# Optimization experiments

Measured on AMD Instinct MI355X. Metric: run time of the kernel, lower is better.

## Reference

```python
import jax, jax.numpy as jnp
import numpy as np

B, T, IN, H, HORIZON = 1024, 256, 128, 128, 24


def setup_inputs() -> dict:
    key = jax.random.key(0)
    ks = jax.random.split(key, 10)
    def init(k, shape, fan_in):
        return jax.random.normal(k, shape, jnp.float32) / np.sqrt(fan_in)
    return {
        "x": jax.random.normal(ks[0], (B, T, IN), jnp.float32),
        # haiku hk.GRU params: w_i [in, 3H], w_h [H, 3H], b [3H]
        "w_i": init(ks[1], (IN, 3 * H), IN),
        "w_h": init(ks[2], (H, 3 * H), H),
        "b": jnp.zeros((3 * H,), jnp.float32),
        # MLP: single Linear H -> 4H (no final activation)
        "mlp_w": init(ks[3], (H, 4 * H), H),
        "mlp_b": jnp.zeros((4 * H,), jnp.float32),
        # fc: Linear(T*4H -> H) after flatten
        "fc_w": init(ks[4], (T * 4 * H, H), T * 4 * H),
        "fc_b": jnp.zeros((H,), jnp.float32),
        # fc_out: Linear(H -> horizon)
        "out_w": init(ks[5], (H, HORIZON), H),
        "out_b": jnp.zeros((HORIZON,), jnp.float32),
    }


def reference(x, w_i, w_h, b, mlp_w, mlp_b, fc_w, fc_b, out_w, out_b):
    h_dim = w_h.shape[0]
    w_h_zr, w_h_a = w_h[:, : 2 * h_dim], w_h[:, 2 * h_dim :]
    b_zr, b_a = b[: 2 * h_dim], b[2 * h_dim :]

    def step(h, xt):  # h: [B,H], xt: [B,IN]  (haiku hk.GRU math)
        gx = xt @ w_i  # [B,3H]
        zr = jax.nn.sigmoid(gx[:, : 2 * h_dim] + h @ w_h_zr + b_zr)
        z, r = zr[:, :h_dim], zr[:, h_dim:]
        a = jnp.tanh(gx[:, 2 * h_dim :] + (r * h) @ w_h_a + b_a)
        h_new = (1.0 - z) * h + z * a
        return h_new, h_new

    h0 = jnp.zeros((x.shape[0], h_dim), x.dtype)
    _, ys = jax.lax.scan(step, h0, jnp.swapaxes(x, 0, 1))  # ys: [T,B,H]
    ys = jnp.swapaxes(ys, 0, 1)  # [B,T,H]
    y = ys @ mlp_w + mlp_b  # [B,T,4H]
    y = y.reshape(x.shape[0], -1)  # [B, T*4H]
    y = y @ fc_w + fc_b  # [B,H]
    return y @ out_w + out_b  # [B,horizon]
```

## Files before the change

### kernel.cpp

```cpp
#include <hip/hip_runtime.h>
#include <hip/hip_bf16.h>

typedef __bf16 bf16x8 __attribute__((ext_vector_type(8)));
typedef float f32x4 __attribute__((ext_vector_type(4)));

#define MFMA16(A, B, C) __builtin_amdgcn_mfma_f32_16x16x32_bf16((A), (B), (C), 0, 0, 0)

namespace {
constexpr int kT = 256, kIN = 128, kHZ = 24;
constexpr int kRB = 16;
}

__device__ __forceinline__ float fsig(float v) {
  float e = __builtin_amdgcn_exp2f(-1.44269504088896340736f * v);
  return __builtin_amdgcn_rcpf(1.0f + e);
}
__device__ __forceinline__ float ftanh(float v) {
  float e = __builtin_amdgcn_exp2f(2.88539008177792681472f * v);
  return 1.0f - 2.0f * __builtin_amdgcn_rcpf(e + 1.0f);
}

__global__ __launch_bounds__(256, 1) void gru_main(
    const float* __restrict__ x, const float* __restrict__ w_i,
    const float* __restrict__ w_h, const float* __restrict__ bias,
    const __bf16* __restrict__ Nfrag, const float* __restrict__ cvec,
    float* __restrict__ out)
{
  const int tid = threadIdx.x;
  const int w = tid >> 6;
  const int l = tid & 63;
  const int lrow = l & 15;
  const int lg = l >> 4;
  const int b0 = blockIdx.x * kRB;

  __shared__ float h_f32[16][132];
  __shared__ float zbuf[16][132];
  __shared__ __align__(16) __bf16 h_bf[16 * 128];
  __shared__ __align__(16) __bf16 rh_bf[16 * 128];
  __shared__ __align__(16) float red[4][64][4];

  for (int i = tid; i < 16 * 132; i += 256) { ((float*)h_f32)[i] = 0.0f; ((float*)zbuf)[i] = 0.0f; }
  for (int i = tid; i < 16 * 128; i += 256) { h_bf[i] = (__bf16)0.0f; rh_bf[i] = (__bf16)0.0f; }

  bf16x8 Wzr[8][4];
  bf16x8 Wa[8][2];
#pragma unroll
  for (int kc = 0; kc < 8; ++kc) {
#pragma unroll
    for (int nt = 0; nt < 4; ++nt) {
      const int col = w * 64 + nt * 16 + lrow;
      bf16x8 f;
#pragma unroll
      for (int e = 0; e < 8; ++e) {
        const int k = kc * 32 + lg * 8 + e;
        const float v = (k < 128) ? w_i[k * 384 + col] : w_h[(k - 128) * 384 + col];
        f[e] = (__bf16)v;
      }
      Wzr[kc][nt] = f;
    }
  }
#pragma unroll
  for (int kc = 0; kc < 8; ++kc) {
#pragma unroll
    for (int nt = 0; nt < 2; ++nt) {
      const int col = 256 + w * 32 + nt * 16 + lrow;
      bf16x8 f;
#pragma unroll
      for (int e = 0; e < 8; ++e) {
        const int k = kc * 32 + lg * 8 + e;
        const float v = (k < 128) ? w_i[k * 384 + col] : w_h[(k - 128) * 384 + col];
        f[e] = (__bf16)v;
      }
      Wa[kc][nt] = f;
    }
  }

  float bz[4], ba[2];
#pragma unroll
  for (int nt = 0; nt < 4; ++nt) bz[nt] = bias[w * 64 + nt * 16 + lrow];
#pragma unroll
  for (int nt = 0; nt < 2; ++nt) ba[nt] = bias[256 + w * 32 + nt * 16 + lrow];

  const int kcA = (w & 2);
  const __bf16* nbase = Nfrag + (size_t)(w & 1) * 512 + (size_t)l * 8;

  const float* xbase = x + ((size_t)(b0 + lrow)) * kT * kIN + lg * 8;

  f32x4 oacc = {0.f, 0.f, 0.f, 0.f};
  bf16x8 nfA, nfB;
#pragma unroll
  for (int e = 0; e < 8; ++e) { nfA[e] = (__bf16)0.0f; nfB[e] = (__bf16)0.0f; }
  bf16x8 xf[4], hf[4], rf[4];
  float4 xpre[8];

#pragma unroll
  for (int kc = 0; kc < 4; ++kc) {
    const float4* p = (const float4*)(xbase + kc * 32);
    xpre[2 * kc] = p[0];
    xpre[2 * kc + 1] = p[1];
  }
#pragma unroll
  for (int kc = 0; kc < 4; ++kc) {
    bf16x8 f;
    f[0] = (__bf16)xpre[2*kc].x;   f[1] = (__bf16)xpre[2*kc].y;
    f[2] = (__bf16)xpre[2*kc].z;   f[3] = (__bf16)xpre[2*kc].w;
    f[4] = (__bf16)xpre[2*kc+1].x; f[5] = (__bf16)xpre[2*kc+1].y;
    f[6] = (__bf16)xpre[2*kc+1].z; f[7] = (__bf16)xpre[2*kc+1].w;
    xf[kc] = f;
  }

  __syncthreads();

#pragma unroll 1
  for (int t = 0; t < kT; ++t) {
#pragma unroll
    for (int kc = 0; kc < 4; ++kc) {
      const int idx = (lrow * 128 + kc * 32 + lg * 8) ^ ((lrow & 7) << 3);
      hf[kc] = *(const bf16x8*)(h_bf + idx);
    }
    if (t > 0) {
      bf16x8 hA, hB;
      if (w & 2) { hA = hf[2]; hB = hf[3]; } else { hA = hf[0]; hB = hf[1]; }
      oacc = MFMA16(hA, nfA, oacc);
      oacc = MFMA16(hB, nfB, oacc);
    }
    {
      const __bf16* np = nbase + (size_t)t * 4096 + (size_t)kcA * 1024;
      nfA = *(const bf16x8*)(np);
      nfB = *(const bf16x8*)(np + 1024);
    }
    {
      const int tn = (t < kT - 1) ? (t + 1) : t;
#pragma unroll
      for (int kc = 0; kc < 4; ++kc) {
        const float4* p = (const float4*)(xbase + (size_t)tn * kIN + kc * 32);
        xpre[2 * kc] = p[0];
        xpre[2 * kc + 1] = p[1];
      }
    }
    f32x4 acc1[4];
#pragma unroll
    for (int nt = 0; nt < 4; ++nt) { f32x4 a = {bz[nt], bz[nt], bz[nt], bz[nt]}; acc1[nt] = a; }
#pragma unroll
    for (int kc = 0; kc < 4; ++kc) {
#pragma unroll
      for (int nt = 0; nt < 4; ++nt) acc1[nt] = MFMA16(xf[kc], Wzr[kc][nt], acc1[nt]);
    }
#pragma unroll
    for (int kc = 0; kc < 4; ++kc) {
#pragma unroll
      for (int nt = 0; nt < 4; ++nt) acc1[nt] = MFMA16(hf[kc], Wzr[kc + 4][nt], acc1[nt]);
    }
    if (w < 2) {
#pragma unroll
      for (int nt = 0; nt < 4; ++nt) {
#pragma unroll
        for (int r = 0; r < 4; ++r) {
          const int row = lg * 4 + r;
          const int col = w * 64 + nt * 16 + lrow;
          zbuf[row][col] = fsig(acc1[nt][r]);
        }
      }
    } else {
#pragma unroll
      for (int nt = 0; nt < 4; ++nt) {
#pragma unroll
        for (int r = 0; r < 4; ++r) {
          const int row = lg * 4 + r;
          const int cr = (w - 2) * 64 + nt * 16 + lrow;
          const float s = fsig(acc1[nt][r]);
          const float rh = s * h_f32[row][cr];
          rh_bf[(row * 128 + cr) ^ ((row & 7) << 3)] = (__bf16)rh;
        }
      }
    }
    __syncthreads();
#pragma unroll
    for (int kc = 0; kc < 4; ++kc) {
      const int idx = (lrow * 128 + kc * 32 + lg * 8) ^ ((lrow & 7) << 3);
      rf[kc] = *(const bf16x8*)(rh_bf + idx);
    }
    f32x4 acc2[2];
#pragma unroll
    for (int nt = 0; nt < 2; ++nt) { f32x4 a = {ba[nt], ba[nt], ba[nt], ba[nt]}; acc2[nt] = a; }
#pragma unroll
    for (int kc = 0; kc < 4; ++kc) {
#pragma unroll
      for (int nt = 0; nt < 2; ++nt) acc2[nt] = MFMA16(xf[kc], Wa[kc][nt], acc2[nt]);
    }
#pragma unroll
    for (int kc = 0; kc < 4; ++kc) {
#pragma unroll
      for (int nt = 0; nt < 2; ++nt) acc2[nt] = MFMA16(rf[kc], Wa[kc + 4][nt], acc2[nt]);
    }
#pragma unroll
    for (int kc = 0; kc < 4; ++kc) {
      bf16x8 f;
      f[0] = (__bf16)xpre[2*kc].x;   f[1] = (__bf16)xpre[2*kc].y;
      f[2] = (__bf16)xpre[2*kc].z;   f[3] = (__bf16)xpre[2*kc].w;
      f[4] = (__bf16)xpre[2*kc+1].x; f[5] = (__bf16)xpre[2*kc+1].y;
      f[6] = (__bf16)xpre[2*kc+1].z; f[7] = (__bf16)xpre[2*kc+1].w;
      xf[kc] = f;
    }
#pragma unroll
    for (int nt = 0; nt < 2; ++nt) {
#pragma unroll
      for (int r = 0; r < 4; ++r) {
        const int row = lg * 4 + r;
        const int col = w * 32 + nt * 16 + lrow;
        const float a = ftanh(acc2[nt][r]);
        const float hold = h_f32[row][col];
        const float z = zbuf[row][col];
        const float hn = fmaf(z, a - hold, hold);
        h_f32[row][col] = hn;
        h_bf[(row * 128 + col) ^ ((row & 7) << 3)] = (__bf16)hn;
      }
    }
    __syncthreads();
  }

#pragma unroll
  for (int kc = 0; kc < 4; ++kc) {
    const int idx = (lrow * 128 + kc * 32 + lg * 8) ^ ((lrow & 7) << 3);
    hf[kc] = *(const bf16x8*)(h_bf + idx);
  }
  {
    bf16x8 hA, hB;
    if (w & 2) { hA = hf[2]; hB = hf[3]; } else { hA = hf[0]; hB = hf[1]; }
    oacc = MFMA16(hA, nfA, oacc);
    oacc = MFMA16(hB, nfB, oacc);
  }
  *(f32x4*)(&red[w][l][0]) = oacc;
  __syncthreads();
  if (w < 2) {
#pragma unroll
    for (int r = 0; r < 4; ++r) {
      const int row = lg * 4 + r;
      const int col = w * 16 + lrow;
      if (col < kHZ) {
        const float v = red[w][l][r] + red[w + 2][l][r] + cvec[col];
        out[(size_t)(b0 + row) * kHZ + col] = v;
      }
    }
  }
}

__global__ __launch_bounds__(256) void nprep(
    const float* __restrict__ mlp_w, const float* __restrict__ fc_w,
    const float* __restrict__ out_w, __bf16* __restrict__ Nfrag)
{
  const int t = blockIdx.x;
  const int tid = threadIdx.x;
  __shared__ __align__(16) float Q[512 * 24];
  __shared__ __align__(16) float obuf[4096];

  float* ow = obuf;
  for (int i = tid; i < 128 * 24; i += 256) ow[i] = out_w[i];
  __syncthreads();

  for (int i = tid; i < 512; i += 256) {
    const float* rowp = fc_w + ((size_t)t * 512 + i) * 128;
    float q[24];
#pragma unroll
    for (int j = 0; j < 24; ++j) q[j] = 0.0f;
    auto acc_m = [&](float rv, int m) {
      const float4* owp = (const float4*)(ow + m * 24);
      const float4 o0 = owp[0], o1 = owp[1], o2 = owp[2];
      const float4 o3 = owp[3], o4 = owp[4], o5 = owp[5];
      q[0]  = fmaf(rv, o0.x, q[0]);  q[1]  = fmaf(rv, o0.y, q[1]);
      q[2]  = fmaf(rv, o0.z, q[2]);  q[3]  = fmaf(rv, o0.w, q[3]);
      q[4]  = fmaf(rv, o1.x, q[4]);  q[5]  = fmaf(rv, o1.y, q[5]);
      q[6]  = fmaf(rv, o1.z, q[6]);  q[7]  = fmaf(rv, o1.w, q[7]);
      q[8]  = fmaf(rv, o2.x, q[8]);  q[9]  = fmaf(rv, o2.y, q[9]);
      q[10] = fmaf(rv, o2.z, q[10]); q[11] = fmaf(rv, o2.w, q[11]);
      q[12] = fmaf(rv, o3.x, q[12]); q[13] = fmaf(rv, o3.y, q[13]);
      q[14] = fmaf(rv, o3.z, q[14]); q[15] = fmaf(rv, o3.w, q[15]);
      q[16] = fmaf(rv, o4.x, q[16]); q[17] = fmaf(rv, o4.y, q[17]);
      q[18] = fmaf(rv, o4.z, q[18]); q[19] = fmaf(rv, o4.w, q[19]);
      q[20] = fmaf(rv, o5.x, q[20]); q[21] = fmaf(rv, o5.y, q[21]);
      q[22] = fmaf(rv, o5.z, q[22]); q[23] = fmaf(rv, o5.w, q[23]);
    };
#pragma unroll 4
    for (int m4 = 0; m4 < 32; ++m4) {
      const float4 rv = *(const float4*)(rowp + m4 * 4);
      acc_m(rv.x, m4 * 4 + 0);
      acc_m(rv.y, m4 * 4 + 1);
      acc_m(rv.z, m4 * 4 + 2);
      acc_m(rv.w, m4 * 4 + 3);
    }
#pragma unroll
    for (int j = 0; j < 24; ++j) Q[i * 24 + j] = q[j];
  }
  __syncthreads();

  {
    const int i = tid & 127;
    const int jh = tid >> 7;
    const float* mrow = mlp_w + (size_t)i * 512;
    float q[12];
#pragma unroll
    for (int j = 0; j < 12; ++j) q[j] = 0.0f;
    auto acc_k = [&](float mv, int k) {
      const float* qrow = Q + (size_t)k * 24 + jh * 12;
      const float4 q0 = *(const float4*)(qrow);
      const float4 q1 = *(const float4*)(qrow + 4);
      const float4 q2 = *(const float4*)(qrow + 8);
      q[0]  = fmaf(mv, q0.x, q[0]);  q[1]  = fmaf(mv, q0.y, q[1]);
      q[2]  = fmaf(mv, q0.z, q[2]);  q[3]  = fmaf(mv, q0.w, q[3]);
      q[4]  = fmaf(mv, q1.x, q[4]);  q[5]  = fmaf(mv, q1.y, q[5]);
      q[6]  = fmaf(mv, q1.z, q[6]);  q[7]  = fmaf(mv, q1.w, q[7]);
      q[8]  = fmaf(mv, q2.x, q[8]);  q[9]  = fmaf(mv, q2.y, q[9]);
      q[10] = fmaf(mv, q2.z, q[10]); q[11] = fmaf(mv, q2.w, q[11]);
    };
#pragma unroll 2
    for (int k4 = 0; k4 < 128; ++k4) {
      const float4 mv = *(const float4*)(mrow + k4 * 4);
      acc_k(mv.x, k4 * 4 + 0);
      acc_k(mv.y, k4 * 4 + 1);
      acc_k(mv.z, k4 * 4 + 2);
      acc_k(mv.w, k4 * 4 + 3);
    }
    float* Nb = obuf;
#pragma unroll
    for (int j = 0; j < 12; ++j) Nb[i * 32 + jh * 12 + j] = q[j];
  }
  for (int idx = tid; idx < 128 * 8; idx += 256) obuf[(idx >> 3) * 32 + 24 + (idx & 7)] = 0.0f;
  __syncthreads();

  {
    const float* Nb = obuf;
#pragma unroll
    for (int u = 0; u < 16; ++u) {
      const int f = tid * 16 + u;
      const int e = f & 7;
      const int lane = (f >> 3) & 63;
      const int nt = (f >> 9) & 1;
      const int kc = f >> 10;
      const int k = kc * 32 + (lane >> 4) * 8 + e;
      const int colj = nt * 16 + (lane & 15);
      Nfrag[(size_t)t * 4096 + f] = (__bf16)Nb[k * 32 + colj];
    }
  }
}

__global__ __launch_bounds__(256) void bias_partial(
    const float* __restrict__ mlp_b, const float* __restrict__ fc_w,
    float* __restrict__ partial)
{
  const int r0 = blockIdx.x;
  const int tid = threadIdx.x;
  const int m = tid & 127;
  const int g = tid >> 7;
  __shared__ int anynz;
  if (tid == 0) anynz = 0;
  __syncthreads();
  {
    int nz = 0;
    for (int i = tid; i < 512; i += 256) nz |= (mlp_b[i] != 0.0f) ? 1 : 0;
    if (nz) atomicOr(&anynz, 1);
  }
  __syncthreads();
  float acc = 0.0f;
  if (anynz) {
    for (int i = g; i < 512; i += 2)
      acc = fmaf(mlp_b[i], fc_w[((size_t)r0 * 512 + i) * 128 + m], acc);
  }
  __shared__ float sred[2][128];
  sred[g][m] = acc;
  __syncthreads();
  if (g == 0) partial[r0 * 128 + m] = sred[0][m] + sred[1][m];
}

__global__ __launch_bounds__(128) void bias_final(
    const float* __restrict__ fc_b, const float* __restrict__ out_b,
    const float* __restrict__ out_w, const float* __restrict__ partial,
    float* __restrict__ cvec)
{
  const int m = threadIdx.x;
  float s = fc_b[m];
  for (int r0 = 0; r0 < 256; ++r0) s += partial[r0 * 128 + m];
  __shared__ float sm[128];
  sm[m] = s;
  __syncthreads();
  if (m < kHZ) {
    float c = out_b[m];
    for (int k = 0; k < 128; ++k) c = fmaf(sm[k], out_w[k * kHZ + m], c);
    cvec[m] = c;
  }
}

extern "C" void kernel_launch(void* const* d_in, const int* in_sizes, int n_in,
                              void* d_out, int out_size, void* d_ws, size_t ws_size,
                              hipStream_t stream) {
  (void)in_sizes; (void)n_in; (void)out_size; (void)ws_size;
  const float* x     = (const float*)d_in[0];
  const float* w_i   = (const float*)d_in[1];
  const float* w_h   = (const float*)d_in[2];
  const float* bias  = (const float*)d_in[3];
  const float* mlp_w = (const float*)d_in[4];
  const float* mlp_b = (const float*)d_in[5];
  const float* fc_w  = (const float*)d_in[6];
  const float* fc_b  = (const float*)d_in[7];
  const float* out_w = (const float*)d_in[8];
  const float* out_b = (const float*)d_in[9];
  float* out = (float*)d_out;

  __bf16* Nfrag  = (__bf16*)d_ws;
  float* partial = (float*)((char*)d_ws + (size_t)256 * 4096 * 2);
  float* cvec    = (float*)((char*)d_ws + (size_t)256 * 4096 * 2 + 256 * 128 * 4);

  nprep<<<256, 256, 0, stream>>>(mlp_w, fc_w, out_w, Nfrag);
  bias_partial<<<256, 256, 0, stream>>>(mlp_b, fc_w, partial);
  bias_final<<<1, 128, 0, stream>>>(fc_b, out_b, out_w, partial, cvec);
  gru_main<<<64, 256, 0, stream>>>(x, w_i, w_h, bias, Nfrag, cvec, out);
}
```

Before: 715.2 us.

## Split GRU recurrence across 8 waves per block and use lighter LDS barriers

Doubles the workgroup from 4 to 8 wavefronts so each wave computes half as many gate columns per timestep. This shortens the serial per-step MFMA chain on the latency-bound recurrence, and the output projection is split four ways across k-chunks and reduced at the end. The __syncthreads calls inside the step loop are replaced by an explicit lgkmcnt wait plus s_barrier. In exchange, each step synchronises more waves, and every wave still loads the full h and x fragments, so redundant LDS and global traffic grows.

```diff
diff --git a/kernel.cpp b/kernel.cpp
--- a/kernel.cpp
+++ b/kernel.cpp
@@ -5,6 +5,11 @@
 typedef float f32x4 __attribute__((ext_vector_type(4)));
 
 #define MFMA16(A, B, C) __builtin_amdgcn_mfma_f32_16x16x32_bf16((A), (B), (C), 0, 0, 0)
+
+#define BARRIER_LDS() do { \
+    asm volatile("s_waitcnt lgkmcnt(0)" ::: "memory"); \
+    __builtin_amdgcn_s_barrier(); \
+  } while (0)
 
 namespace {
 constexpr int kT = 256, kIN = 128, kHZ = 24;
@@ -20,7 +25,7 @@
   return 1.0f - 2.0f * __builtin_amdgcn_rcpf(e + 1.0f);
 }
 
-__global__ __launch_bounds__(256, 1) void gru_main(
+__global__ __launch_bounds__(512, 2) void gru_main(
     const float* __restrict__ x, const float* __restrict__ w_i,
     const float* __restrict__ w_h, const float* __restrict__ bias,
     const __bf16* __restrict__ Nfrag, const float* __restrict__ cvec,
@@ -37,18 +42,18 @@
   __shared__ float zbuf[16][132];
   __shared__ __align__(16) __bf16 h_bf[16 * 128];
   __shared__ __align__(16) __bf16 rh_bf[16 * 128];
-  __shared__ __align__(16) float red[4][64][4];
-
-  for (int i = tid; i < 16 * 132; i += 256) { ((float*)h_f32)[i] = 0.0f; ((float*)zbuf)[i] = 0.0f; }
-  for (int i = tid; i < 16 * 128; i += 256) { h_bf[i] = (__bf16)0.0f; rh_bf[i] = (__bf16)0.0f; }
-
-  bf16x8 Wzr[8][4];
-  bf16x8 Wa[8][2];
+  __shared__ __align__(16) float red[8][64][4];
+
+  for (int i = tid; i < 16 * 132; i += 512) { ((float*)h_f32)[i] = 0.0f; ((float*)zbuf)[i] = 0.0f; }
+  for (int i = tid; i < 16 * 128; i += 512) { h_bf[i] = (__bf16)0.0f; rh_bf[i] = (__bf16)0.0f; }
+
+  bf16x8 Wzr[8][2];
+  bf16x8 Wa[8];
 #pragma unroll
   for (int kc = 0; kc < 8; ++kc) {
 #pragma unroll
-    for (int nt = 0; nt < 4; ++nt) {
-      const int col = w * 64 + nt * 16 + lrow;
+    for (int nt = 0; nt < 2; ++nt) {
+      const int col = w * 32 + nt * 16 + lrow;
       bf16x8 f;
 #pragma unroll
       for (int e = 0; e < 8; ++e) {
@@ -61,35 +66,32 @@
   }
 #pragma unroll
   for (int kc = 0; kc < 8; ++kc) {
-#pragma unroll
-    for (int nt = 0; nt < 2; ++nt) {
-      const int col = 256 + w * 32 + nt * 16 + lrow;
-      bf16x8 f;
-#pragma unroll
-      for (int e = 0; e < 8; ++e) {
-        const int k = kc * 32 + lg * 8 + e;
-        const float v = (k < 128) ? w_i[k * 384 + col] : w_h[(k - 128) * 384 + col];
-        f[e] = (__bf16)v;
-      }
-      Wa[kc][nt] = f;
-    }
-  }
-
-  float bz[4], ba[2];
-#pragma unroll
-  for (int nt = 0; nt < 4; ++nt) bz[nt] = bias[w * 64 + nt * 16 + lrow];
-#pragma unroll
-  for (int nt = 0; nt < 2; ++nt) ba[nt] = bias[256 + w * 32 + nt * 16 + lrow];
-
-  const int kcA = (w & 2);
-  const __bf16* nbase = Nfrag + (size_t)(w & 1) * 512 + (size_t)l * 8;
+    const int col = 256 + w * 16 + lrow;
+    bf16x8 f;
+#pragma unroll
+    for (int e = 0; e < 8; ++e) {
+      const int k = kc * 32 + lg * 8 + e;
+      const float v = (k < 128) ? w_i[k * 384 + col] : w_h[(k - 128) * 384 + col];
+      f[e] = (__bf16)v;
+    }
+    Wa[kc] = f;
+  }
+
+  float bz[2], ba;
+#pragma unroll
+  for (int nt = 0; nt < 2; ++nt) bz[nt] = bias[w * 32 + nt * 16 + lrow];
+  ba = bias[256 + w * 16 + lrow];
+
+  const int kcA = w & 3;
+  const int ntA = w >> 2;
+  const __bf16* nbase = Nfrag + (size_t)kcA * 1024 + (size_t)ntA * 512 + (size_t)l * 8;
 
   const float* xbase = x + ((size_t)(b0 + lrow)) * kT * kIN + lg * 8;
 
   f32x4 oacc = {0.f, 0.f, 0.f, 0.f};
-  bf16x8 nfA, nfB;
-#pragma unroll
-  for (int e = 0; e < 8; ++e) { nfA[e] = (__bf16)0.0f; nfB[e] = (__bf16)0.0f; }
+  bf16x8 nf;
+#pragma unroll
+  for (int e = 0; e < 8; ++e) nf[e] = (__bf16)0.0f;
   bf16x8 xf[4], hf[4], rf[4];
   float4 xpre[8];
 
@@ -113,22 +115,6 @@
 
 #pragma unroll 1
   for (int t = 0; t < kT; ++t) {
-#pragma unroll
-    for (int kc = 0; kc < 4; ++kc) {
-      const int idx = (lrow * 128 + kc * 32 + lg * 8) ^ ((lrow & 7) << 3);
-      hf[kc] = *(const bf16x8*)(h_bf + idx);
-    }
-    if (t > 0) {
-      bf16x8 hA, hB;
-      if (w & 2) { hA = hf[2]; hB = hf[3]; } else { hA = hf[0]; hB = hf[1]; }
-      oacc = MFMA16(hA, nfA, oacc);
-      oacc = MFMA16(hB, nfB, oacc);
-    }
-    {
-      const __bf16* np = nbase + (size_t)t * 4096 + (size_t)kcA * 1024;
-      nfA = *(const bf16x8*)(np);
-      nfB = *(const bf16x8*)(np + 1024);
-    }
     {
       const int tn = (t < kT - 1) ? (t + 1) : t;
 #pragma unroll
@@ -138,61 +124,62 @@
         xpre[2 * kc + 1] = p[1];
       }
     }
-    f32x4 acc1[4];
-#pragma unroll
-    for (int nt = 0; nt < 4; ++nt) { f32x4 a = {bz[nt], bz[nt], bz[nt], bz[nt]}; acc1[nt] = a; }
-#pragma unroll
-    for (int kc = 0; kc < 4; ++kc) {
-#pragma unroll
-      for (int nt = 0; nt < 4; ++nt) acc1[nt] = MFMA16(xf[kc], Wzr[kc][nt], acc1[nt]);
-    }
-#pragma unroll
-    for (int kc = 0; kc < 4; ++kc) {
-#pragma unroll
-      for (int nt = 0; nt < 4; ++nt) acc1[nt] = MFMA16(hf[kc], Wzr[kc + 4][nt], acc1[nt]);
-    }
-    if (w < 2) {
-#pragma unroll
-      for (int nt = 0; nt < 4; ++nt) {
+#pragma unroll
+    for (int kc = 0; kc < 4; ++kc) {
+      const int idx = (lrow * 128 + kc * 32 + lg * 8) ^ ((lrow & 7) << 3);
+      hf[kc] = *(const bf16x8*)(h_bf + idx);
+    }
+    if (t > 0) {
+      oacc = MFMA16(hf[kcA], nf, oacc);
+    }
+    nf = *(const bf16x8*)(nbase + (size_t)t * 4096);
+    f32x4 acc1[2];
+#pragma unroll
+    for (int nt = 0; nt < 2; ++nt) { f32x4 a = {bz[nt], bz[nt], bz[nt], bz[nt]}; acc1[nt] = a; }
+#pragma unroll
+    for (int kc = 0; kc < 4; ++kc) {
+#pragma unroll
+      for (int nt = 0; nt < 2; ++nt) acc1[nt] = MFMA16(xf[kc], Wzr[kc][nt], acc1[nt]);
+    }
+#pragma unroll
+    for (int kc = 0; kc < 4; ++kc) {
+#pragma unroll
+      for (int nt = 0; nt < 2; ++nt) acc1[nt] = MFMA16(hf[kc], Wzr[kc + 4][nt], acc1[nt]);
+    }
+    if (w < 4) {
+#pragma unroll
+      for (int nt = 0; nt < 2; ++nt) {
 #pragma unroll
         for (int r = 0; r < 4; ++r) {
           const int row = lg * 4 + r;
-          const int col = w * 64 + nt * 16 + lrow;
+          const int col = w * 32 + nt * 16 + lrow;
           zbuf[row][col] = fsig(acc1[nt][r]);
         }
       }
     } else {
 #pragma unroll
-      for (int nt = 0; nt < 4; ++nt) {
+      for (int nt = 0; nt < 2; ++nt) {
 #pragma unroll
         for (int r = 0; r < 4; ++r) {
           const int row = lg * 4 + r;
-          const int cr = (w - 2) * 64 + nt * 16 + lrow;
+          const int cr = (w - 4) * 32 + nt * 16 + lrow;
           const float s = fsig(acc1[nt][r]);
           const float rh = s * h_f32[row][cr];
           rh_bf[(row * 128 + cr) ^ ((row & 7) << 3)] = (__bf16)rh;
         }
       }
     }
-    __syncthreads();
+    BARRIER_LDS();
 #pragma unroll
     for (int kc = 0; kc < 4; ++kc) {
       const int idx = (lrow * 128 + kc * 32 + lg * 8) ^ ((lrow & 7) << 3);
       rf[kc] = *(const bf16x8*)(rh_bf + idx);
     }
-    f32x4 acc2[2];
-#pragma unroll
-    for (int nt = 0; nt < 2; ++nt) { f32x4 a = {ba[nt], ba[nt], ba[nt], ba[nt]}; acc2[nt] = a; }
-#pragma unroll
-    for (int kc = 0; kc < 4; ++kc) {
-#pragma unroll
-      for (int nt = 0; nt < 2; ++nt) acc2[nt] = MFMA16(xf[kc], Wa[kc][nt], acc2[nt]);
-    }
-#pragma unroll
-    for (int kc = 0; kc < 4; ++kc) {
-#pragma unroll
-      for (int nt = 0; nt < 2; ++nt) acc2[nt] = MFMA16(rf[kc], Wa[kc + 4][nt], acc2[nt]);
-    }
+    f32x4 acc2 = {ba, ba, ba, ba};
+#pragma unroll
+    for (int kc = 0; kc < 4; ++kc) acc2 = MFMA16(xf[kc], Wa[kc], acc2);
+#pragma unroll
+    for (int kc = 0; kc < 4; ++kc) acc2 = MFMA16(rf[kc], Wa[kc + 4], acc2);
 #pragma unroll
     for (int kc = 0; kc < 4; ++kc) {
       bf16x8 f;
@@ -202,13 +189,12 @@
       f[6] = (__bf16)xpre[2*kc+1].z; f[7] = (__bf16)xpre[2*kc+1].w;
       xf[kc] = f;
     }
-#pragma unroll
-    for (int nt = 0; nt < 2; ++nt) {
+    {
 #pragma unroll
       for (int r = 0; r < 4; ++r) {
         const int row = lg * 4 + r;
-        const int col = w * 32 + nt * 16 + lrow;
-        const float a = ftanh(acc2[nt][r]);
+        const int col = w * 16 + lrow;
+        const float a = ftanh(acc2[r]);
         const float hold = h_f32[row][col];
         const float z = zbuf[row][col];
         const float hn = fmaf(z, a - hold, hold);
@@ -216,29 +202,24 @@
         h_bf[(row * 128 + col) ^ ((row & 7) << 3)] = (__bf16)hn;
       }
     }
-    __syncthreads();
-  }
-
-#pragma unroll
-  for (int kc = 0; kc < 4; ++kc) {
-    const int idx = (lrow * 128 + kc * 32 + lg * 8) ^ ((lrow & 7) << 3);
-    hf[kc] = *(const bf16x8*)(h_bf + idx);
-  }
+    BARRIER_LDS();
+  }
+
   {
-    bf16x8 hA, hB;
-    if (w & 2) { hA = hf[2]; hB = hf[3]; } else { hA = hf[0]; hB = hf[1]; }
-    oacc = MFMA16(hA, nfA, oacc);
-    oacc = MFMA16(hB, nfB, oacc);
+    const int idx = (lrow * 128 + kcA * 32 + lg * 8) ^ ((lrow & 7) << 3);
+    bf16x8 hlast = *(const bf16x8*)(h_bf + idx);
+    oacc = MFMA16(hlast, nf, oacc);
   }
   *(f32x4*)(&red[w][l][0]) = oacc;
   __syncthreads();
-  if (w < 2) {
+  if ((w & 3) == 0) {
 #pragma unroll
     for (int r = 0; r < 4; ++r) {
       const int row = lg * 4 + r;
-      const int col = w * 16 + lrow;
+      const int col = ntA * 16 + lrow;
       if (col < kHZ) {
-        const float v = red[w][l][r] + red[w + 2][l][r] + cvec[col];
+        const float v = red[w][l][r] + red[w + 1][l][r] + red[w + 2][l][r] +
+                        red[w + 3][l][r] + cvec[col];
         out[(size_t)(b0 + row) * kHZ + col] = v;
       }
     }
@@ -412,5 +393,5 @@
   nprep<<<256, 256, 0, stream>>>(mlp_w, fc_w, out_w, Nfrag);
   bias_partial<<<256, 256, 0, stream>>>(mlp_b, fc_w, partial);
   bias_final<<<1, 128, 0, stream>>>(fc_b, out_b, out_w, partial, cvec);
-  gru_main<<<64, 256, 0, stream>>>(x, w_i, w_h, bias, Nfrag, cvec, out);
-}
+  gru_main<<<64, 512, 0, stream>>>(x, w_i, w_h, bias, Nfrag, cvec, out);
+}
```

New measurement: 912.7 us. 1.28x slower.

## Keep GRU state in registers, split gate columns per wave, prepack x to bf16 fragments

Applied to the files above, without the earlier changes.

Each wave now owns matching z, r and candidate columns, so the hidden state and update gate stay in registers instead of fp32 shared buffers. The z/r column split is reworked, and the output projection is spread across all four waves with a four-way reduction. A new xprep kernel converts x into bf16 MFMA fragment layout ahead of time so the recurrent loop does plain vector loads without conversion; it only runs when the workspace is large enough. Barriers become a raw LDS waitcnt plus s_barrier, and the N-fragment loads are double-buffered one step ahead. The extra prepass adds a full read of x and a workspace write.

```diff
diff --git a/kernel.cpp b/kernel.cpp
--- a/kernel.cpp
+++ b/kernel.cpp
@@ -6,9 +6,13 @@
 
 #define MFMA16(A, B, C) __builtin_amdgcn_mfma_f32_16x16x32_bf16((A), (B), (C), 0, 0, 0)
 
+#define BARRIER_LDS() do { \
+    asm volatile("s_waitcnt lgkmcnt(0)" ::: "memory"); \
+    __builtin_amdgcn_s_barrier(); \
+  } while (0)
+
 namespace {
 constexpr int kT = 256, kIN = 128, kHZ = 24;
-constexpr int kRB = 16;
 }
 
 __device__ __forceinline__ float fsig(float v) {
@@ -20,26 +24,24 @@
   return 1.0f - 2.0f * __builtin_amdgcn_rcpf(e + 1.0f);
 }
 
+template<int XF>
 __global__ __launch_bounds__(256, 1) void gru_main(
-    const float* __restrict__ x, const float* __restrict__ w_i,
-    const float* __restrict__ w_h, const float* __restrict__ bias,
-    const __bf16* __restrict__ Nfrag, const float* __restrict__ cvec,
-    float* __restrict__ out)
+    const float* __restrict__ x, const __bf16* __restrict__ xfrag,
+    const float* __restrict__ w_i, const float* __restrict__ w_h,
+    const float* __restrict__ bias, const __bf16* __restrict__ Nfrag,
+    const float* __restrict__ cvec, float* __restrict__ out)
 {
   const int tid = threadIdx.x;
   const int w = tid >> 6;
   const int l = tid & 63;
   const int lrow = l & 15;
   const int lg = l >> 4;
-  const int b0 = blockIdx.x * kRB;
-
-  __shared__ float h_f32[16][132];
-  __shared__ float zbuf[16][132];
+  const int b0 = blockIdx.x * 16;
+
   __shared__ __align__(16) __bf16 h_bf[16 * 128];
   __shared__ __align__(16) __bf16 rh_bf[16 * 128];
-  __shared__ __align__(16) float red[4][64][4];
-
-  for (int i = tid; i < 16 * 132; i += 256) { ((float*)h_f32)[i] = 0.0f; ((float*)zbuf)[i] = 0.0f; }
+  __shared__ __align__(16) float red[4][2][64][4];
+
   for (int i = tid; i < 16 * 128; i += 256) { h_bf[i] = (__bf16)0.0f; rh_bf[i] = (__bf16)0.0f; }
 
   bf16x8 Wzr[8][4];
@@ -48,7 +50,8 @@
   for (int kc = 0; kc < 8; ++kc) {
 #pragma unroll
     for (int nt = 0; nt < 4; ++nt) {
-      const int col = w * 64 + nt * 16 + lrow;
+      const int col = (nt < 2) ? (w * 32 + nt * 16 + lrow)
+                               : (128 + w * 32 + (nt - 2) * 16 + lrow);
       bf16x8 f;
 #pragma unroll
       for (int e = 0; e < 8; ++e) {
@@ -75,62 +78,52 @@
     }
   }
 
-  float bz[4], ba[2];
-#pragma unroll
-  for (int nt = 0; nt < 4; ++nt) bz[nt] = bias[w * 64 + nt * 16 + lrow];
-#pragma unroll
-  for (int nt = 0; nt < 2; ++nt) ba[nt] = bias[256 + w * 32 + nt * 16 + lrow];
-
-  const int kcA = (w & 2);
-  const __bf16* nbase = Nfrag + (size_t)(w & 1) * 512 + (size_t)l * 8;
-
+  float bz[2], br[2], ba[2];
+#pragma unroll
+  for (int nt = 0; nt < 2; ++nt) {
+    bz[nt] = bias[w * 32 + nt * 16 + lrow];
+    br[nt] = bias[128 + w * 32 + nt * 16 + lrow];
+    ba[nt] = bias[256 + w * 32 + nt * 16 + lrow];
+  }
+
+  float hreg[2][4] = {{0.f,0.f,0.f,0.f},{0.f,0.f,0.f,0.f}};
+  float zreg[2][4];
+
+  const __bf16* nl = Nfrag + (size_t)w * 1024 + (size_t)l * 8;
+  const __bf16* xl = xfrag + (size_t)blockIdx.x * kT * 2048 + (size_t)l * 8;
   const float* xbase = x + ((size_t)(b0 + lrow)) * kT * kIN + lg * 8;
 
-  f32x4 oacc = {0.f, 0.f, 0.f, 0.f};
-  bf16x8 nfA, nfB;
-#pragma unroll
-  for (int e = 0; e < 8; ++e) { nfA[e] = (__bf16)0.0f; nfB[e] = (__bf16)0.0f; }
-  bf16x8 xf[4], hf[4], rf[4];
+  f32x4 oacc[2] = {{0.f,0.f,0.f,0.f},{0.f,0.f,0.f,0.f}};
+  bf16x8 xf[4], xfn[4], hf[4], rf[4], nf[2], nfn[2];
   float4 xpre[8];
 
-#pragma unroll
-  for (int kc = 0; kc < 4; ++kc) {
-    const float4* p = (const float4*)(xbase + kc * 32);
-    xpre[2 * kc] = p[0];
-    xpre[2 * kc + 1] = p[1];
-  }
-#pragma unroll
-  for (int kc = 0; kc < 4; ++kc) {
-    bf16x8 f;
-    f[0] = (__bf16)xpre[2*kc].x;   f[1] = (__bf16)xpre[2*kc].y;
-    f[2] = (__bf16)xpre[2*kc].z;   f[3] = (__bf16)xpre[2*kc].w;
-    f[4] = (__bf16)xpre[2*kc+1].x; f[5] = (__bf16)xpre[2*kc+1].y;
-    f[6] = (__bf16)xpre[2*kc+1].z; f[7] = (__bf16)xpre[2*kc+1].w;
-    xf[kc] = f;
-  }
+  if (XF) {
+#pragma unroll
+    for (int kc = 0; kc < 4; ++kc) xf[kc] = *(const bf16x8*)(xl + kc * 512);
+  } else {
+#pragma unroll
+    for (int kc = 0; kc < 4; ++kc) {
+      const float4* p = (const float4*)(xbase + kc * 32);
+      const float4 a = p[0], b = p[1];
+      bf16x8 f;
+      f[0]=(__bf16)a.x; f[1]=(__bf16)a.y; f[2]=(__bf16)a.z; f[3]=(__bf16)a.w;
+      f[4]=(__bf16)b.x; f[5]=(__bf16)b.y; f[6]=(__bf16)b.z; f[7]=(__bf16)b.w;
+      xf[kc] = f;
+    }
+  }
+  nfn[0] = *(const bf16x8*)(nl);
+  nfn[1] = *(const bf16x8*)(nl + 512);
 
   __syncthreads();
 
 #pragma unroll 1
   for (int t = 0; t < kT; ++t) {
-#pragma unroll
-    for (int kc = 0; kc < 4; ++kc) {
-      const int idx = (lrow * 128 + kc * 32 + lg * 8) ^ ((lrow & 7) << 3);
-      hf[kc] = *(const bf16x8*)(h_bf + idx);
-    }
-    if (t > 0) {
-      bf16x8 hA, hB;
-      if (w & 2) { hA = hf[2]; hB = hf[3]; } else { hA = hf[0]; hB = hf[1]; }
-      oacc = MFMA16(hA, nfA, oacc);
-      oacc = MFMA16(hB, nfB, oacc);
-    }
-    {
-      const __bf16* np = nbase + (size_t)t * 4096 + (size_t)kcA * 1024;
-      nfA = *(const bf16x8*)(np);
-      nfB = *(const bf16x8*)(np + 1024);
-    }
-    {
-      const int tn = (t < kT - 1) ? (t + 1) : t;
+    const int tn = (t < kT - 1) ? (t + 1) : t;
+    if (XF) {
+      const __bf16* xp = xl + (size_t)tn * 2048;
+#pragma unroll
+      for (int kc = 0; kc < 4; ++kc) xfn[kc] = *(const bf16x8*)(xp + kc * 512);
+    } else {
 #pragma unroll
       for (int kc = 0; kc < 4; ++kc) {
         const float4* p = (const float4*)(xbase + (size_t)tn * kIN + kc * 32);
@@ -138,9 +131,27 @@
         xpre[2 * kc + 1] = p[1];
       }
     }
+#pragma unroll
+    for (int kc = 0; kc < 4; ++kc) {
+      const int idx = (lrow * 128 + kc * 32 + lg * 8) ^ ((lrow & 7) << 3);
+      hf[kc] = *(const bf16x8*)(h_bf + idx);
+    }
+    if (t > 0) {
+      oacc[0] = MFMA16(hf[w], nf[0], oacc[0]);
+      oacc[1] = MFMA16(hf[w], nf[1], oacc[1]);
+    }
+    nf[0] = nfn[0]; nf[1] = nfn[1];
+    if (t < kT - 1) {
+      const __bf16* np = nl + (size_t)(t + 1) * 4096;
+      nfn[0] = *(const bf16x8*)(np);
+      nfn[1] = *(const bf16x8*)(np + 512);
+    }
     f32x4 acc1[4];
 #pragma unroll
-    for (int nt = 0; nt < 4; ++nt) { f32x4 a = {bz[nt], bz[nt], bz[nt], bz[nt]}; acc1[nt] = a; }
+    for (int nt = 0; nt < 2; ++nt) {
+      f32x4 a = {bz[nt], bz[nt], bz[nt], bz[nt]}; acc1[nt] = a;
+      f32x4 b = {br[nt], br[nt], br[nt], br[nt]}; acc1[2 + nt] = b;
+    }
 #pragma unroll
     for (int kc = 0; kc < 4; ++kc) {
 #pragma unroll
@@ -151,30 +162,19 @@
 #pragma unroll
       for (int nt = 0; nt < 4; ++nt) acc1[nt] = MFMA16(hf[kc], Wzr[kc + 4][nt], acc1[nt]);
     }
-    if (w < 2) {
-#pragma unroll
-      for (int nt = 0; nt < 4; ++nt) {
-#pragma unroll
-        for (int r = 0; r < 4; ++r) {
-          const int row = lg * 4 + r;
-          const int col = w * 64 + nt * 16 + lrow;
-          zbuf[row][col] = fsig(acc1[nt][r]);
-        }
-      }
-    } else {
-#pragma unroll
-      for (int nt = 0; nt < 4; ++nt) {
-#pragma unroll
-        for (int r = 0; r < 4; ++r) {
-          const int row = lg * 4 + r;
-          const int cr = (w - 2) * 64 + nt * 16 + lrow;
-          const float s = fsig(acc1[nt][r]);
-          const float rh = s * h_f32[row][cr];
-          rh_bf[(row * 128 + cr) ^ ((row & 7) << 3)] = (__bf16)rh;
-        }
-      }
-    }
-    __syncthreads();
+#pragma unroll
+    for (int nt = 0; nt < 2; ++nt) {
+#pragma unroll
+      for (int j = 0; j < 4; ++j) {
+        zreg[nt][j] = fsig(acc1[nt][j]);
+        const float rr = fsig(acc1[2 + nt][j]);
+        const float rh = rr * hreg[nt][j];
+        const int row = lg * 4 + j;
+        const int col = w * 32 + nt * 16 + lrow;
+        rh_bf[(row * 128 + col) ^ ((row & 7) << 3)] = (__bf16)rh;
+      }
+    }
+    BARRIER_LDS();
 #pragma unroll
     for (int kc = 0; kc < 4; ++kc) {
       const int idx = (lrow * 128 + kc * 32 + lg * 8) ^ ((lrow & 7) << 3);
@@ -193,56 +193,72 @@
 #pragma unroll
       for (int nt = 0; nt < 2; ++nt) acc2[nt] = MFMA16(rf[kc], Wa[kc + 4][nt], acc2[nt]);
     }
-#pragma unroll
-    for (int kc = 0; kc < 4; ++kc) {
-      bf16x8 f;
-      f[0] = (__bf16)xpre[2*kc].x;   f[1] = (__bf16)xpre[2*kc].y;
-      f[2] = (__bf16)xpre[2*kc].z;   f[3] = (__bf16)xpre[2*kc].w;
-      f[4] = (__bf16)xpre[2*kc+1].x; f[5] = (__bf16)xpre[2*kc+1].y;
-      f[6] = (__bf16)xpre[2*kc+1].z; f[7] = (__bf16)xpre[2*kc+1].w;
-      xf[kc] = f;
+    if (!XF) {
+#pragma unroll
+      for (int kc = 0; kc < 4; ++kc) {
+        bf16x8 f;
+        f[0]=(__bf16)xpre[2*kc].x;   f[1]=(__bf16)xpre[2*kc].y;
+        f[2]=(__bf16)xpre[2*kc].z;   f[3]=(__bf16)xpre[2*kc].w;
+        f[4]=(__bf16)xpre[2*kc+1].x; f[5]=(__bf16)xpre[2*kc+1].y;
+        f[6]=(__bf16)xpre[2*kc+1].z; f[7]=(__bf16)xpre[2*kc+1].w;
+        xfn[kc] = f;
+      }
     }
 #pragma unroll
     for (int nt = 0; nt < 2; ++nt) {
 #pragma unroll
-      for (int r = 0; r < 4; ++r) {
-        const int row = lg * 4 + r;
+      for (int j = 0; j < 4; ++j) {
+        const float a = ftanh(acc2[nt][j]);
+        const float hn = fmaf(zreg[nt][j], a - hreg[nt][j], hreg[nt][j]);
+        hreg[nt][j] = hn;
+        const int row = lg * 4 + j;
         const int col = w * 32 + nt * 16 + lrow;
-        const float a = ftanh(acc2[nt][r]);
-        const float hold = h_f32[row][col];
-        const float z = zbuf[row][col];
-        const float hn = fmaf(z, a - hold, hold);
-        h_f32[row][col] = hn;
         h_bf[(row * 128 + col) ^ ((row & 7) << 3)] = (__bf16)hn;
       }
     }
-    __syncthreads();
-  }
-
-#pragma unroll
-  for (int kc = 0; kc < 4; ++kc) {
-    const int idx = (lrow * 128 + kc * 32 + lg * 8) ^ ((lrow & 7) << 3);
-    hf[kc] = *(const bf16x8*)(h_bf + idx);
-  }
+#pragma unroll
+    for (int kc = 0; kc < 4; ++kc) xf[kc] = xfn[kc];
+    BARRIER_LDS();
+  }
+
   {
-    bf16x8 hA, hB;
-    if (w & 2) { hA = hf[2]; hB = hf[3]; } else { hA = hf[0]; hB = hf[1]; }
-    oacc = MFMA16(hA, nfA, oacc);
-    oacc = MFMA16(hB, nfB, oacc);
-  }
-  *(f32x4*)(&red[w][l][0]) = oacc;
+    const int idx = (lrow * 128 + w * 32 + lg * 8) ^ ((lrow & 7) << 3);
+    bf16x8 hlast = *(const bf16x8*)(h_bf + idx);
+    oacc[0] = MFMA16(hlast, nf[0], oacc[0]);
+    oacc[1] = MFMA16(hlast, nf[1], oacc[1]);
+  }
+  *(f32x4*)(&red[w][0][l][0]) = oacc[0];
+  *(f32x4*)(&red[w][1][l][0]) = oacc[1];
   __syncthreads();
   if (w < 2) {
-#pragma unroll
-    for (int r = 0; r < 4; ++r) {
-      const int row = lg * 4 + r;
-      const int col = w * 16 + lrow;
+    const int nt = w;
+#pragma unroll
+    for (int j = 0; j < 4; ++j) {
+      const int row = lg * 4 + j;
+      const int col = nt * 16 + lrow;
       if (col < kHZ) {
-        const float v = red[w][l][r] + red[w + 2][l][r] + cvec[col];
+        const float v = red[0][nt][l][j] + red[1][nt][l][j] +
+                        red[2][nt][l][j] + red[3][nt][l][j] + cvec[col];
         out[(size_t)(b0 + row) * kHZ + col] = v;
       }
     }
   }
+}
+
+__global__ __launch_bounds__(256) void xprep(
+    const float* __restrict__ x, __bf16* __restrict__ xfrag)
+{
+  const int bg = blockIdx.x, t = blockIdx.y;
+  const int tid = threadIdx.x;
+  const int kc = tid >> 6, l = tid & 63;
+  const int row = l & 15, lgx = l >> 4;
+  const float* src = x + (((size_t)(bg * 16 + row)) * kT + t) * kIN + kc * 32 + lgx * 8;
+  const float4 a = ((const float4*)src)[0];
+  const float4 b = ((const float4*)src)[1];
+  bf16x8 f;
+  f[0]=(__bf16)a.x; f[1]=(__bf16)a.y; f[2]=(__bf16)a.z; f[3]=(__bf16)a.w;
+  f[4]=(__bf16)b.x; f[5]=(__bf16)b.y; f[6]=(__bf16)b.z; f[7]=(__bf16)b.w;
+  *(bf16x8*)(xfrag + ((size_t)bg * kT + t) * 2048 + (size_t)tid * 8) = f;
 }
 
 __global__ __launch_bounds__(256) void nprep(
@@ -392,7 +408,7 @@
 extern "C" void kernel_launch(void* const* d_in, const int* in_sizes, int n_in,
                               void* d_out, int out_size, void* d_ws, size_t ws_size,
                               hipStream_t stream) {
-  (void)in_sizes; (void)n_in; (void)out_size; (void)ws_size;
+  (void)in_sizes; (void)n_in; (void)out_size;
   const float* x     = (const float*)d_in[0];
   const float* w_i   = (const float*)d_in[1];
   const float* w_h   = (const float*)d_in[2];
@@ -405,12 +421,23 @@
   const float* out_b = (const float*)d_in[9];
   float* out = (float*)d_out;
 
+  const size_t nfrag_b   = (size_t)256 * 4096 * 2;
+  const size_t partial_b = (size_t)256 * 128 * 4;
+  const size_t cvec_b    = 4096;
+  const size_t xfrag_b   = (size_t)64 * 256 * 2048 * 2;
   __bf16* Nfrag  = (__bf16*)d_ws;
-  float* partial = (float*)((char*)d_ws + (size_t)256 * 4096 * 2);
-  float* cvec    = (float*)((char*)d_ws + (size_t)256 * 4096 * 2 + 256 * 128 * 4);
+  float* partial = (float*)((char*)d_ws + nfrag_b);
+  float* cvec    = (float*)((char*)d_ws + nfrag_b + partial_b);
+  __bf16* xfrag  = (__bf16*)((char*)d_ws + nfrag_b + partial_b + cvec_b);
+  const bool use_xf = ws_size >= nfrag_b + partial_b + cvec_b + xfrag_b;
 
   nprep<<<256, 256, 0, stream>>>(mlp_w, fc_w, out_w, Nfrag);
   bias_partial<<<256, 256, 0, stream>>>(mlp_b, fc_w, partial);
   bias_final<<<1, 128, 0, stream>>>(fc_b, out_b, out_w, partial, cvec);
-  gru_main<<<64, 256, 0, stream>>>(x, w_i, w_h, bias, Nfrag, cvec, out);
-}
+  if (use_xf) {
+    xprep<<<dim3(64, 256), 256, 0, stream>>>(x, xfrag);
+    gru_main<1><<<64, 256, 0, stream>>>(x, xfrag, w_i, w_h, bias, Nfrag, cvec, out);
+  } else {
+    gru_main<0><<<64, 256, 0, stream>>>(x, xfrag, w_i, w_h, bias, Nfrag, cvec, out);
+  }
+}
```

After: 816.8 us. 14.2% more time.
